# Kernel tuning notes

Measured on AMD Instinct MI355X. Metric: run time of the kernel, lower is better.

Reference implementation:

```python
import jax, jax.numpy as jnp
import numpy as np

NS_ITERS = 15
EPS = 1e-6


def _sqrtm(x):
    """Newton-Schulz matrix square root, 15 fixed iterations (Lin & Maji)."""
    dim = x.shape[0]
    norm = jnp.linalg.norm(x)  # Frobenius norm
    Y = x / norm
    I = jnp.eye(dim, dtype=x.dtype)
    Z = I
    for _ in range(NS_ITERS):
        T = 0.5 * (3.0 * I - Z @ Y)
        Y = Y @ T
        Z = T @ Z
    return Y * jnp.sqrt(norm)


def _gram(X):
    a, b = X.shape
    return (X @ X.T + EPS * jnp.eye(a, dtype=X.dtype)) / b


def setup_inputs() -> dict:
    key = jax.random.key(0)
    k1, k2 = jax.random.split(key)
    inp = jax.random.normal(k1, (1, 512, 256, 256), dtype=jnp.float32)
    tgt = jax.random.normal(k2, (1, 512, 256, 256), dtype=jnp.float32)
    return {"input": inp, "target_feature": tgt}


def reference(input, target_feature):
    a, b, c, d = input.shape
    n = a * b
    # --- target statistics (precomputed in __init__ of the torch module) ---
    Xt = target_feature.reshape(n, c * d)
    Mt = Xt.mean(axis=1)                     # [n]
    Gt = _gram(Xt - Mt[:, None])             # [n, n]
    sqrt_Gt = _sqrtm(Gt)                     # [n, n]
    # --- current statistics ---
    X = input.reshape(n, c * d)
    M = X.mean(axis=1)
    G = _gram(X - M[:, None])
    sqrt_G = _sqrtm(G)
    # mse(reduction='sum') on means + Bures/Wasserstein SPD distance
    loss = jnp.sum((M - Mt) ** 2)
    loss = loss + jnp.trace(G + Gt) - 2.0 * jnp.trace(sqrt_G @ sqrt_Gt)
    return loss / b
```

## Files before the change

### kernel.cpp

```cpp
#include <hip/hip_runtime.h>
#include <math.h>

#define KDIM 65536
#define MATF 262144
#define EPSG 1e-6

using bf16x8 = __attribute__((ext_vector_type(8))) __bf16;
using f32x4  = __attribute__((ext_vector_type(4))) float;


__global__ __launch_bounds__(256) void k_means(const float* __restrict__ X,
                                               const float* __restrict__ Xt,
                                               float* __restrict__ M) {
  const int row = blockIdx.x, inp = blockIdx.y;
  const float4* p = (const float4*)((inp ? Xt : X) + (size_t)row * KDIM);
  double s = 0.0;
  for (int i = threadIdx.x; i < KDIM / 4; i += 256) {
    float4 v = p[i];
    s += (double)v.x + (double)v.y + (double)v.z + (double)v.w;
  }
  __shared__ double sm[256];
  sm[threadIdx.x] = s;
  __syncthreads();
  for (int o = 128; o > 0; o >>= 1) {
    if (threadIdx.x < o) sm[threadIdx.x] += sm[threadIdx.x + o];
    __syncthreads();
  }
  if (threadIdx.x == 0) M[inp * 512 + row] = (float)(sm[0] * (1.0 / KDIM));
}

__device__ __forceinline__ void cvt8(float4 a, float4 b, bf16x8& hi, bf16x8& lo) {
  float f[8] = {a.x, a.y, a.z, a.w, b.x, b.y, b.z, b.w};
#pragma unroll
  for (int e = 0; e < 8; ++e) {
    __bf16 h = (__bf16)f[e];
    hi[e] = h;
    lo[e] = (__bf16)(f[e] - (float)h);
  }
}

__global__ __launch_bounds__(256, 2) void k_gram(const float* __restrict__ X,
                                                 const float* __restrict__ Xt,
                                                 float* __restrict__ Gp, int nk) {
  int rem = blockIdx.x, ti = 0;
  while (rem >= 4 - ti) { rem -= 4 - ti; ++ti; }
  const int tj = ti + rem;
  const int chunk = blockIdx.y, inp = blockIdx.z;
  const int chunkv = KDIM / nk;
  const float* __restrict__ A = inp ? Xt : X;
  float* __restrict__ C = Gp + ((size_t)(inp * nk + chunk)) * MATF;
  const bool diag = (ti == tj);

  __shared__ bf16x8 AhV[512], AlV[512], BhV[512], BlV[512];

  const int t = threadIdx.x;
  const int srow = t & 127, skh = t >> 7;
  const int sbase = ((srow >> 4) << 6) + (skh << 5) + (srow & 15);

  const float* pa = A + (size_t)(ti * 128 + srow) * KDIM + (size_t)chunk * chunkv + skh * 16;
  const float* pb = A + (size_t)(tj * 128 + srow) * KDIM + (size_t)chunk * chunkv + skh * 16;

  const int wave = t >> 6, lane = t & 63;
  const int wy = (wave >> 1) * 64, wx = (wave & 1) * 64;

  f32x4 acc[4][4];
#pragma unroll
  for (int i = 0; i < 4; ++i)
#pragma unroll
    for (int j = 0; j < 4; ++j) acc[i][j] = (f32x4){0.f, 0.f, 0.f, 0.f};

  float4 ra0 = *(const float4*)(pa);
  float4 ra1 = *(const float4*)(pa + 4);
  float4 ra2 = *(const float4*)(pa + 8);
  float4 ra3 = *(const float4*)(pa + 12);
  float4 rb0 = {}, rb1 = {}, rb2 = {}, rb3 = {};
  if (!diag) {
    rb0 = *(const float4*)(pb);
    rb1 = *(const float4*)(pb + 4);
    rb2 = *(const float4*)(pb + 8);
    rb3 = *(const float4*)(pb + 12);
  }

  for (int ks = 0; ks < chunkv; ks += 32) {
    {
      bf16x8 h, l;
      cvt8(ra0, ra1, h, l); AhV[sbase] = h; AlV[sbase] = l;
      cvt8(ra2, ra3, h, l); AhV[sbase + 16] = h; AlV[sbase + 16] = l;
      if (!diag) {
        cvt8(rb0, rb1, h, l); BhV[sbase] = h; BlV[sbase] = l;
        cvt8(rb2, rb3, h, l); BhV[sbase + 16] = h; BlV[sbase + 16] = l;
      }
    }
    __syncthreads();
    if (ks + 32 < chunkv) {
      ra0 = *(const float4*)(pa + ks + 32);
      ra1 = *(const float4*)(pa + ks + 36);
      ra2 = *(const float4*)(pa + ks + 40);
      ra3 = *(const float4*)(pa + ks + 44);
      if (!diag) {
        rb0 = *(const float4*)(pb + ks + 32);
        rb1 = *(const float4*)(pb + ks + 36);
        rb2 = *(const float4*)(pb + ks + 40);
        rb3 = *(const float4*)(pb + ks + 44);
      }
    }
    const bf16x8* __restrict__ Bh = diag ? AhV : BhV;
    const bf16x8* __restrict__ Bl = diag ? AlV : BlV;
    bf16x8 ah[4], al[4], bh[4], bl[4];
#pragma unroll
    for (int g = 0; g < 4; ++g) {
      ah[g] = AhV[((wave >> 1) * 4 + g) * 64 + lane];
      al[g] = AlV[((wave >> 1) * 4 + g) * 64 + lane];
      bh[g] = Bh[((wave & 1) * 4 + g) * 64 + lane];
      bl[g] = Bl[((wave & 1) * 4 + g) * 64 + lane];
    }
#pragma unroll
    for (int i = 0; i < 4; ++i)
#pragma unroll
      for (int j = 0; j < 4; ++j) {
        acc[i][j] = __builtin_amdgcn_mfma_f32_16x16x32_bf16(ah[i], bh[j], acc[i][j], 0, 0, 0);
        acc[i][j] = __builtin_amdgcn_mfma_f32_16x16x32_bf16(al[i], bh[j], acc[i][j], 0, 0, 0);
        acc[i][j] = __builtin_amdgcn_mfma_f32_16x16x32_bf16(ah[i], bl[j], acc[i][j], 0, 0, 0);
      }
    __syncthreads();
  }
  const int r4 = (lane >> 4) * 4, fc = lane & 15;
#pragma unroll
  for (int i = 0; i < 4; ++i) {
    const int grow = ti * 128 + wy + i * 16 + r4;
#pragma unroll
    for (int j = 0; j < 4; ++j) {
      const int gcol = tj * 128 + wx + j * 16 + fc;
#pragma unroll
      for (int r = 0; r < 4; ++r)
        C[(size_t)(grow + r) * 512 + gcol] = acc[i][j][r];
    }
  }
}

__global__ __launch_bounds__(256) void k_gfin(const float* __restrict__ Gp,
                                              const float* __restrict__ M,
                                              float* __restrict__ G,
                                              double* __restrict__ S, int nk) {
  const int inp = blockIdx.y;
  const int idx = blockIdx.x * 256 + threadIdx.x;
  const int i = idx >> 9, j = idx & 511;
  double n2 = 0.0, tr = 0.0;
  float* g = G + (size_t)inp * MATF;
  if (i <= j) {
    double sum = 0.0;
    const float* p = Gp + (size_t)inp * nk * MATF + idx;
    for (int c = 0; c < nk; ++c) sum += (double)p[(size_t)c * MATF];
    sum -= 65536.0 * (double)M[inp * 512 + i] * (double)M[inp * 512 + j];
    if (i == j) sum += EPSG;
    float v = (float)(sum * (1.0 / 65536.0));
    g[idx] = v;
    if (i < j) { g[(size_t)j * 512 + i] = v; n2 = 2.0 * (double)v * (double)v; }
    else       { n2 = (double)v * (double)v; tr = (double)v; }
  }
  __shared__ double s1[256], s2[256];
  s1[threadIdx.x] = n2; s2[threadIdx.x] = tr;
  __syncthreads();
  for (int o = 128; o > 0; o >>= 1) {
    if (threadIdx.x < o) { s1[threadIdx.x] += s1[threadIdx.x + o]; s2[threadIdx.x] += s2[threadIdx.x + o]; }
    __syncthreads();
  }
  if (threadIdx.x == 0) { atomicAdd(&S[inp], s1[0]); atomicAdd(&S[2 + inp], s2[0]); }
}

__global__ __launch_bounds__(256) void k_nsinit(const float* __restrict__ G,
                                                float* __restrict__ Y0,
                                                float* __restrict__ Z1,
                                                const double* __restrict__ S) {
  const int inp = blockIdx.y;
  const int idx = blockIdx.x * 256 + threadIdx.x;
  const float norm = (float)sqrt(S[inp]);
  const float y = G[(size_t)inp * MATF + idx] / norm;
  Y0[(size_t)inp * MATF + idx] = y;
  Z1[(size_t)inp * MATF + idx] = ((idx >> 9) == (idx & 511)) ? (1.5f - 0.5f * y) : (-0.5f * y);
}

__device__ __forceinline__ void ns_gemm(const float* __restrict__ A,
                                        const float* __restrict__ B,
                                        const float* __restrict__ E,
                                        float* __restrict__ C, int mode) {
  int rem = blockIdx.x, ti = 0;
  while (rem >= 4 - ti) { rem -= 4 - ti; ++ti; }
  const int tj = ti + rem;

  __shared__ bf16x8 AhV[512], AlV[512], BhV[512], BlV[512];

  const int t = threadIdx.x;
  const int srow = t & 127, sko = t >> 7;
  const int sslot = ((srow >> 4) << 6) + (sko << 4) + (srow & 15);

  const float* pa = A + (size_t)(ti * 128 + srow) * 512 + sko * 8;
  const float* pb = B + (size_t)(tj * 128 + srow) * 512 + sko * 8;

  const int wave = t >> 6, lane = t & 63;
  const int wy = (wave >> 2) * 64, wx = (wave & 3) * 32;

  f32x4 acc[4][2];
#pragma unroll
  for (int i = 0; i < 4; ++i)
#pragma unroll
    for (int j = 0; j < 2; ++j) acc[i][j] = (f32x4){0.f, 0.f, 0.f, 0.f};

  float4 ra0 = *(const float4*)(pa), ra1 = *(const float4*)(pa + 4);
  float4 rb0 = *(const float4*)(pb), rb1 = *(const float4*)(pb + 4);

  for (int ks = 0; ks < 512; ks += 32) {
    {
      bf16x8 h, l;
      cvt8(ra0, ra1, h, l); AhV[sslot] = h; AlV[sslot] = l;
      cvt8(rb0, rb1, h, l); BhV[sslot] = h; BlV[sslot] = l;
    }
    __syncthreads();
    if (ks + 32 < 512) {
      ra0 = *(const float4*)(pa + ks + 32); ra1 = *(const float4*)(pa + ks + 36);
      rb0 = *(const float4*)(pb + ks + 32); rb1 = *(const float4*)(pb + ks + 36);
    }
    bf16x8 ah[4], al[4], bh[2], bl[2];
#pragma unroll
    for (int g = 0; g < 4; ++g) {
      ah[g] = AhV[((wy >> 4) + g) * 64 + lane];
      al[g] = AlV[((wy >> 4) + g) * 64 + lane];
    }
#pragma unroll
    for (int g = 0; g < 2; ++g) {
      bh[g] = BhV[((wx >> 4) + g) * 64 + lane];
      bl[g] = BlV[((wx >> 4) + g) * 64 + lane];
    }
#pragma unroll
    for (int i = 0; i < 4; ++i)
#pragma unroll
      for (int j = 0; j < 2; ++j) {
        acc[i][j] = __builtin_amdgcn_mfma_f32_16x16x32_bf16(ah[i], bh[j], acc[i][j], 0, 0, 0);
        acc[i][j] = __builtin_amdgcn_mfma_f32_16x16x32_bf16(al[i], bh[j], acc[i][j], 0, 0, 0);
        acc[i][j] = __builtin_amdgcn_mfma_f32_16x16x32_bf16(ah[i], bl[j], acc[i][j], 0, 0, 0);
      }
    __syncthreads();
  }

  const int r4 = (lane >> 4) * 4, fc = lane & 15;
#pragma unroll
  for (int i = 0; i < 4; ++i) {
    const int grow = ti * 128 + wy + i * 16 + r4;
#pragma unroll
    for (int j = 0; j < 2; ++j) {
      const int gcol = tj * 128 + wx + j * 16 + fc;
      float v[4];
#pragma unroll
      for (int r = 0; r < 4; ++r) v[r] = acc[i][j][r];
      if (mode) {
#pragma unroll
        for (int r = 0; r < 4; ++r)
          v[r] = 1.5f * E[(size_t)(grow + r) * 512 + gcol] - 0.5f * v[r];
      }
#pragma unroll
      for (int r = 0; r < 4; ++r) C[(size_t)(grow + r) * 512 + gcol] = v[r];
      if (ti != tj) {
        float4 mv = make_float4(v[0], v[1], v[2], v[3]);
        *(float4*)&C[(size_t)gcol * 512 + grow] = mv;
      }
    }
  }
}

__global__ __launch_bounds__(512, 2) void k_ns_first(const float* __restrict__ Y0,
                                                     float* __restrict__ Y1) {
  const int mat = blockIdx.y;
  const float* a = Y0 + (size_t)mat * MATF;
  ns_gemm(a, a, a, Y1 + (size_t)mat * MATF, 1);
}

__global__ __launch_bounds__(512, 2) void k_ns_W(const float* __restrict__ Y,
                                                 const float* __restrict__ Z,
                                                 float* __restrict__ W) {
  const int mat = blockIdx.y;
  ns_gemm(Z + (size_t)mat * MATF, Y + (size_t)mat * MATF, nullptr,
          W + (size_t)mat * MATF, 0);
}

__global__ __launch_bounds__(512, 2) void k_ns_YZ(const float* __restrict__ Y,
                                                  const float* __restrict__ Z,
                                                  const float* __restrict__ W,
                                                  float* __restrict__ Yn,
                                                  float* __restrict__ Zn) {
  const int mat = blockIdx.y >> 1, which = blockIdx.y & 1;
  const float* Wp = W + (size_t)mat * MATF;
  if (which == 0) {
    const float* Yp = Y + (size_t)mat * MATF;
    ns_gemm(Yp, Wp, Yp, Yn + (size_t)mat * MATF, 1);
  } else {
    const float* Zp = Z + (size_t)mat * MATF;
    ns_gemm(Wp, Zp, Zp, Zn + (size_t)mat * MATF, 1);
  }
}

__global__ __launch_bounds__(256) void k_cross(const float* __restrict__ Y,
                                               double* __restrict__ S) {
  const float* YA = Y;
  const float* YB = Y + MATF;
  const int base = (blockIdx.x * 256 + threadIdx.x) * 4;
  double s = 0.0;
#pragma unroll
  for (int r = 0; r < 4; ++r) {
    const int id = base + r;
    const int i = id >> 9, j = id & 511;
    s += (double)YA[id] * (double)YB[j * 512 + i];
  }
  __shared__ double sm[256];
  sm[threadIdx.x] = s;
  __syncthreads();
  for (int o = 128; o > 0; o >>= 1) {
    if (threadIdx.x < o) sm[threadIdx.x] += sm[threadIdx.x + o];
    __syncthreads();
  }
  if (threadIdx.x == 0) atomicAdd(&S[4], sm[0]);
}

__global__ __launch_bounds__(256) void k_final(const float* __restrict__ M,
                                               const double* __restrict__ S,
                                               float* __restrict__ out) {
  double s = 0.0;
  for (int i = threadIdx.x; i < 512; i += 256) {
    double d = (double)M[i] - (double)M[512 + i];
    s += d * d;
  }
  __shared__ double sm[256];
  sm[threadIdx.x] = s;
  __syncthreads();
  for (int o = 128; o > 0; o >>= 1) {
    if (threadIdx.x < o) sm[threadIdx.x] += sm[threadIdx.x + o];
    __syncthreads();
  }
  if (threadIdx.x == 0) {
    double scale = sqrt(sqrt(S[0]) * sqrt(S[1]));
    double loss = sm[0] + S[2] + S[3] - 2.0 * scale * S[4];
    out[0] = (float)(loss / 512.0);
  }
}

extern "C" void kernel_launch(void* const* d_in, const int* in_sizes, int n_in,
                              void* d_out, int out_size, void* d_ws, size_t ws_size,
                              hipStream_t stream) {
  const float* X = (const float*)d_in[0];
  const float* Xt = (const float*)d_in[1];
  char* wsb = (char*)d_ws;
  float* Mv = (float*)wsb;
  double* S = (double*)(wsb + 4096);
  float* G = (float*)(wsb + 8192);
  float* big = (float*)(wsb + 8192 + 2 * (size_t)MATF * 4);

  const size_t need32 = 8192 + 2 * (size_t)MATF * 4 + 2 * 32 * (size_t)MATF * 4;
  const int nk = (ws_size >= need32) ? 32 : 16;

  float* Gp = big;
  float* Yb[2] = { big, big + 2 * (size_t)MATF };
  float* Zb[2] = { big + 4 * (size_t)MATF, big + 6 * (size_t)MATF };
  float* W = big + 8 * (size_t)MATF;

  hipMemsetAsync(S, 0, 16 * sizeof(double), stream);
  k_means<<<dim3(512, 2), 256, 0, stream>>>(X, Xt, Mv);
  k_gram<<<dim3(10, nk, 2), 256, 0, stream>>>(X, Xt, Gp, nk);
  k_gfin<<<dim3(1024, 2), 256, 0, stream>>>(Gp, Mv, G, S, nk);
  k_nsinit<<<dim3(1024, 2), 256, 0, stream>>>(G, Yb[0], Zb[1], S);
  k_ns_first<<<dim3(10, 2), 512, 0, stream>>>(Yb[0], Yb[1]);
  int cur = 1;
  for (int it = 1; it < 15; ++it) {
    k_ns_W<<<dim3(10, 2), 512, 0, stream>>>(Yb[cur], Zb[cur], W);
    k_ns_YZ<<<dim3(10, 4), 512, 0, stream>>>(Yb[cur], Zb[cur], W, Yb[1 - cur], Zb[1 - cur]);
    cur ^= 1;
  }
  k_cross<<<dim3(256), 256, 0, stream>>>(Yb[cur], S);
  k_final<<<dim3(1), 256, 0, stream>>>(Mv, S, (float*)d_out);
}
```

Measured before the change: 1.323 ms.

## Fuse Newton-Schulz chain into persistent kernel with grid barriers and 64x64 tiles

Replaces the Gram finalize, NS init, 29 per-step NS GEMM launches, cross-trace and final kernels with one persistent kernel. The kernel synchronises its phases through an atomic-counter grid barrier. GEMM tiles shrink from 128x128 to 64x64, giving 72 or 144 jobs per step instead of 20 or 40 blocks, to use more CUs. This removes launch gaps and raises parallelism. It relies on all blocks being co-resident, and the barrier has a timeout break that could silently desynchronise phases.

```diff
diff --git a/kernel.cpp b/kernel.cpp
--- a/kernel.cpp
+++ b/kernel.cpp
@@ -138,71 +138,47 @@
   }
 }
 
-__global__ __launch_bounds__(256) void k_gfin(const float* __restrict__ Gp,
-                                              const float* __restrict__ M,
-                                              float* __restrict__ G,
-                                              double* __restrict__ S, int nk) {
-  const int inp = blockIdx.y;
-  const int idx = blockIdx.x * 256 + threadIdx.x;
-  const int i = idx >> 9, j = idx & 511;
-  double n2 = 0.0, tr = 0.0;
-  float* g = G + (size_t)inp * MATF;
-  if (i <= j) {
-    double sum = 0.0;
-    const float* p = Gp + (size_t)inp * nk * MATF + idx;
-    for (int c = 0; c < nk; ++c) sum += (double)p[(size_t)c * MATF];
-    sum -= 65536.0 * (double)M[inp * 512 + i] * (double)M[inp * 512 + j];
-    if (i == j) sum += EPSG;
-    float v = (float)(sum * (1.0 / 65536.0));
-    g[idx] = v;
-    if (i < j) { g[(size_t)j * 512 + i] = v; n2 = 2.0 * (double)v * (double)v; }
-    else       { n2 = (double)v * (double)v; tr = (double)v; }
-  }
-  __shared__ double s1[256], s2[256];
-  s1[threadIdx.x] = n2; s2[threadIdx.x] = tr;
+__device__ __forceinline__ void gbar(unsigned* cnt, unsigned target) {
   __syncthreads();
-  for (int o = 128; o > 0; o >>= 1) {
-    if (threadIdx.x < o) { s1[threadIdx.x] += s1[threadIdx.x + o]; s2[threadIdx.x] += s2[threadIdx.x + o]; }
-    __syncthreads();
-  }
-  if (threadIdx.x == 0) { atomicAdd(&S[inp], s1[0]); atomicAdd(&S[2 + inp], s2[0]); }
-}
-
-__global__ __launch_bounds__(256) void k_nsinit(const float* __restrict__ G,
-                                                float* __restrict__ Y0,
-                                                float* __restrict__ Z1,
-                                                const double* __restrict__ S) {
-  const int inp = blockIdx.y;
-  const int idx = blockIdx.x * 256 + threadIdx.x;
-  const float norm = (float)sqrt(S[inp]);
-  const float y = G[(size_t)inp * MATF + idx] / norm;
-  Y0[(size_t)inp * MATF + idx] = y;
-  Z1[(size_t)inp * MATF + idx] = ((idx >> 9) == (idx & 511)) ? (1.5f - 0.5f * y) : (-0.5f * y);
-}
-
-__device__ __forceinline__ void ns_gemm(const float* __restrict__ A,
-                                        const float* __restrict__ B,
-                                        const float* __restrict__ E,
-                                        float* __restrict__ C, int mode) {
-  int rem = blockIdx.x, ti = 0;
-  while (rem >= 4 - ti) { rem -= 4 - ti; ++ti; }
-  const int tj = ti + rem;
-
-  __shared__ bf16x8 AhV[512], AlV[512], BhV[512], BlV[512];
-
+  if (threadIdx.x == 0) {
+    __threadfence();
+    atomicAdd(cnt, 1u);
+    unsigned long long t0 = __builtin_amdgcn_s_memrealtime();
+    while (__hip_atomic_load(cnt, __ATOMIC_RELAXED, __HIP_MEMORY_SCOPE_AGENT) < target) {
+      __builtin_amdgcn_s_sleep(16);
+      if (__builtin_amdgcn_s_memrealtime() - t0 > 2000000ull) break;
+    }
+    __threadfence();
+  }
+  __syncthreads();
+}
+
+__device__ __forceinline__ void tri8(int x, int& ti, int& tj) {
+  int rem = x, i = 0;
+  while (rem >= 8 - i) { rem -= 8 - i; ++i; }
+  ti = i; tj = i + rem;
+}
+
+__device__ __forceinline__ void gemm64(const float* __restrict__ A,
+                                       const float* __restrict__ B,
+                                       const float* __restrict__ E,
+                                       float* __restrict__ C,
+                                       int ti, int tj, int mode,
+                                       bf16x8* AhV, bf16x8* AlV,
+                                       bf16x8* BhV, bf16x8* BlV) {
   const int t = threadIdx.x;
-  const int srow = t & 127, sko = t >> 7;
+  const int srow = t & 63, sko = t >> 6;
   const int sslot = ((srow >> 4) << 6) + (sko << 4) + (srow & 15);
 
-  const float* pa = A + (size_t)(ti * 128 + srow) * 512 + sko * 8;
-  const float* pb = B + (size_t)(tj * 128 + srow) * 512 + sko * 8;
+  const float* pa = A + (size_t)(ti * 64 + srow) * 512 + sko * 8;
+  const float* pb = B + (size_t)(tj * 64 + srow) * 512 + sko * 8;
 
   const int wave = t >> 6, lane = t & 63;
-  const int wy = (wave >> 2) * 64, wx = (wave & 3) * 32;
-
-  f32x4 acc[4][2];
-#pragma unroll
-  for (int i = 0; i < 4; ++i)
+  const int wy = (wave >> 1) * 32, wx = (wave & 1) * 32;
+
+  f32x4 acc[2][2];
+#pragma unroll
+  for (int i = 0; i < 2; ++i)
 #pragma unroll
     for (int j = 0; j < 2; ++j) acc[i][j] = (f32x4){0.f, 0.f, 0.f, 0.f};
 
@@ -220,19 +196,16 @@
       ra0 = *(const float4*)(pa + ks + 32); ra1 = *(const float4*)(pa + ks + 36);
       rb0 = *(const float4*)(pb + ks + 32); rb1 = *(const float4*)(pb + ks + 36);
     }
-    bf16x8 ah[4], al[4], bh[2], bl[2];
-#pragma unroll
-    for (int g = 0; g < 4; ++g) {
+    bf16x8 ah[2], al[2], bh[2], bl[2];
+#pragma unroll
+    for (int g = 0; g < 2; ++g) {
       ah[g] = AhV[((wy >> 4) + g) * 64 + lane];
       al[g] = AlV[((wy >> 4) + g) * 64 + lane];
-    }
-#pragma unroll
-    for (int g = 0; g < 2; ++g) {
       bh[g] = BhV[((wx >> 4) + g) * 64 + lane];
       bl[g] = BlV[((wx >> 4) + g) * 64 + lane];
     }
 #pragma unroll
-    for (int i = 0; i < 4; ++i)
+    for (int i = 0; i < 2; ++i)
 #pragma unroll
       for (int j = 0; j < 2; ++j) {
         acc[i][j] = __builtin_amdgcn_mfma_f32_16x16x32_bf16(ah[i], bh[j], acc[i][j], 0, 0, 0);
@@ -244,11 +217,11 @@
 
   const int r4 = (lane >> 4) * 4, fc = lane & 15;
 #pragma unroll
-  for (int i = 0; i < 4; ++i) {
-    const int grow = ti * 128 + wy + i * 16 + r4;
+  for (int i = 0; i < 2; ++i) {
+    const int grow = ti * 64 + wy + i * 16 + r4;
 #pragma unroll
     for (int j = 0; j < 2; ++j) {
-      const int gcol = tj * 128 + wx + j * 16 + fc;
+      const int gcol = tj * 64 + wx + j * 16 + fc;
       float v[4];
 #pragma unroll
       for (int r = 0; r < 4; ++r) v[r] = acc[i][j][r];
@@ -267,78 +240,147 @@
   }
 }
 
-__global__ __launch_bounds__(512, 2) void k_ns_first(const float* __restrict__ Y0,
-                                                     float* __restrict__ Y1) {
-  const int mat = blockIdx.y;
-  const float* a = Y0 + (size_t)mat * MATF;
-  ns_gemm(a, a, a, Y1 + (size_t)mat * MATF, 1);
-}
-
-__global__ __launch_bounds__(512, 2) void k_ns_W(const float* __restrict__ Y,
-                                                 const float* __restrict__ Z,
-                                                 float* __restrict__ W) {
-  const int mat = blockIdx.y;
-  ns_gemm(Z + (size_t)mat * MATF, Y + (size_t)mat * MATF, nullptr,
-          W + (size_t)mat * MATF, 0);
-}
-
-__global__ __launch_bounds__(512, 2) void k_ns_YZ(const float* __restrict__ Y,
-                                                  const float* __restrict__ Z,
-                                                  const float* __restrict__ W,
-                                                  float* __restrict__ Yn,
-                                                  float* __restrict__ Zn) {
-  const int mat = blockIdx.y >> 1, which = blockIdx.y & 1;
-  const float* Wp = W + (size_t)mat * MATF;
-  if (which == 0) {
-    const float* Yp = Y + (size_t)mat * MATF;
-    ns_gemm(Yp, Wp, Yp, Yn + (size_t)mat * MATF, 1);
-  } else {
-    const float* Zp = Z + (size_t)mat * MATF;
-    ns_gemm(Wp, Zp, Zp, Zn + (size_t)mat * MATF, 1);
-  }
-}
-
-__global__ __launch_bounds__(256) void k_cross(const float* __restrict__ Y,
-                                               double* __restrict__ S) {
-  const float* YA = Y;
-  const float* YB = Y + MATF;
-  const int base = (blockIdx.x * 256 + threadIdx.x) * 4;
-  double s = 0.0;
-#pragma unroll
-  for (int r = 0; r < 4; ++r) {
-    const int id = base + r;
-    const int i = id >> 9, j = id & 511;
-    s += (double)YA[id] * (double)YB[j * 512 + i];
-  }
-  __shared__ double sm[256];
-  sm[threadIdx.x] = s;
-  __syncthreads();
-  for (int o = 128; o > 0; o >>= 1) {
-    if (threadIdx.x < o) sm[threadIdx.x] += sm[threadIdx.x + o];
-    __syncthreads();
-  }
-  if (threadIdx.x == 0) atomicAdd(&S[4], sm[0]);
-}
-
-__global__ __launch_bounds__(256) void k_final(const float* __restrict__ M,
-                                               const double* __restrict__ S,
-                                               float* __restrict__ out) {
-  double s = 0.0;
-  for (int i = threadIdx.x; i < 512; i += 256) {
-    double d = (double)M[i] - (double)M[512 + i];
-    s += d * d;
-  }
-  __shared__ double sm[256];
-  sm[threadIdx.x] = s;
-  __syncthreads();
-  for (int o = 128; o > 0; o >>= 1) {
-    if (threadIdx.x < o) sm[threadIdx.x] += sm[threadIdx.x + o];
-    __syncthreads();
-  }
-  if (threadIdx.x == 0) {
-    double scale = sqrt(sqrt(S[0]) * sqrt(S[1]));
-    double loss = sm[0] + S[2] + S[3] - 2.0 * scale * S[4];
-    out[0] = (float)(loss / 512.0);
+__global__ __launch_bounds__(256, 2) void k_all(const float* Gp,
+                                                const float* __restrict__ M,
+                                                float* __restrict__ Gm,
+                                                double* __restrict__ S,
+                                                unsigned* __restrict__ bar,
+                                                float* big,
+                                                float* __restrict__ out, int nk) {
+  __shared__ bf16x8 AhV[256], AlV[256], BhV[256], BlV[256];
+  __shared__ double red[256];
+  __shared__ float s_nrm[2];
+
+  const int t = threadIdx.x;
+  const int b = blockIdx.x;
+  const int gsz = gridDim.x;
+  unsigned tgt = 0;
+
+  float* Ya = big;
+  float* Yb = big + 2 * (size_t)MATF;
+  float* Za = big + 4 * (size_t)MATF;
+  float* Zb = big + 6 * (size_t)MATF;
+  float* W  = big + 8 * (size_t)MATF;
+
+  {
+    double n2[2] = {0.0, 0.0}, trc[2] = {0.0, 0.0};
+    for (int e = b * 256 + t; e < 2 * MATF; e += gsz * 256) {
+      const int inp = e >> 18, idx = e & (MATF - 1);
+      const int i = idx >> 9, j = idx & 511;
+      if (i <= j) {
+        double sum = 0.0;
+        const float* p = Gp + (size_t)inp * nk * MATF + idx;
+        for (int c = 0; c < nk; ++c) sum += (double)p[(size_t)c * MATF];
+        sum -= 65536.0 * (double)M[inp * 512 + i] * (double)M[inp * 512 + j];
+        if (i == j) sum += EPSG;
+        float v = (float)(sum * (1.0 / 65536.0));
+        Gm[e] = v;
+        if (i < j) { Gm[((size_t)inp << 18) + j * 512 + i] = v; n2[inp] += 2.0 * (double)v * (double)v; }
+        else       { n2[inp] += (double)v * (double)v; trc[inp] += (double)v; }
+      }
+    }
+#pragma unroll
+    for (int inp = 0; inp < 2; ++inp) {
+      red[t] = n2[inp]; __syncthreads();
+      for (int o = 128; o > 0; o >>= 1) { if (t < o) red[t] += red[t + o]; __syncthreads(); }
+      if (t == 0) atomicAdd(&S[inp], red[0]);
+      __syncthreads();
+      red[t] = trc[inp]; __syncthreads();
+      for (int o = 128; o > 0; o >>= 1) { if (t < o) red[t] += red[t + o]; __syncthreads(); }
+      if (t == 0) atomicAdd(&S[2 + inp], red[0]);
+      __syncthreads();
+    }
+  }
+  gbar(bar, tgt += gsz);
+
+  {
+    if (t < 2)
+      s_nrm[t] = (float)sqrt(__hip_atomic_load(&S[t], __ATOMIC_RELAXED, __HIP_MEMORY_SCOPE_AGENT));
+    __syncthreads();
+    for (int e = b * 256 + t; e < 2 * MATF; e += gsz * 256) {
+      const int inp = e >> 18, idx = e & (MATF - 1);
+      const float y = Gm[e] / s_nrm[inp];
+      Ya[e] = y;
+      Za[e] = ((idx >> 9) == (idx & 511)) ? (1.5f - 0.5f * y) : (-0.5f * y);
+    }
+  }
+  gbar(bar, tgt += gsz);
+
+  for (int job = b; job < 72; job += gsz) {
+    const int mat = job >= 36;
+    int ti, tj; tri8(job - mat * 36, ti, tj);
+    const float* a = Ya + (size_t)mat * MATF;
+    gemm64(a, a, a, Yb + (size_t)mat * MATF, ti, tj, 1, AhV, AlV, BhV, BlV);
+  }
+  gbar(bar, tgt += gsz);
+
+  float *Y = Yb, *Z = Za, *Yn = Ya, *Zn = Zb;
+  for (int it = 1; it < 15; ++it) {
+    for (int job = b; job < 72; job += gsz) {
+      const int mat = job >= 36;
+      int ti, tj; tri8(job - mat * 36, ti, tj);
+      gemm64(Z + (size_t)mat * MATF, Y + (size_t)mat * MATF, nullptr,
+             W + (size_t)mat * MATF, ti, tj, 0, AhV, AlV, BhV, BlV);
+    }
+    gbar(bar, tgt += gsz);
+    for (int job = b; job < 144; job += gsz) {
+      if (job < 72) {
+        const int mat = job >= 36;
+        int ti, tj; tri8(job - mat * 36, ti, tj);
+        gemm64(Y + (size_t)mat * MATF, W + (size_t)mat * MATF, Y + (size_t)mat * MATF,
+               Yn + (size_t)mat * MATF, ti, tj, 1, AhV, AlV, BhV, BlV);
+      } else {
+        const int jb = job - 72;
+        const int mat = jb >= 36;
+        int ti, tj; tri8(jb - mat * 36, ti, tj);
+        gemm64(W + (size_t)mat * MATF, Z + (size_t)mat * MATF, Z + (size_t)mat * MATF,
+               Zn + (size_t)mat * MATF, ti, tj, 1, AhV, AlV, BhV, BlV);
+      }
+    }
+    gbar(bar, tgt += gsz);
+    float* tmp;
+    tmp = Y; Y = Yn; Yn = tmp;
+    tmp = Z; Z = Zn; Zn = tmp;
+  }
+
+  {
+    double s = 0.0;
+    for (int id = b * 256 + t; id < MATF; id += gsz * 256) {
+      const int i = id >> 9, j = id & 511;
+      s += (double)Y[id] * (double)Y[MATF + j * 512 + i];
+    }
+    red[t] = s;
+    __syncthreads();
+    for (int o = 128; o > 0; o >>= 1) {
+      if (t < o) red[t] += red[t + o];
+      __syncthreads();
+    }
+    if (t == 0) atomicAdd(&S[4], red[0]);
+  }
+  gbar(bar, tgt += gsz);
+
+  if (b == 0) {
+    double s = 0.0;
+    for (int i = t; i < 512; i += 256) {
+      double d = (double)M[i] - (double)M[512 + i];
+      s += d * d;
+    }
+    red[t] = s;
+    __syncthreads();
+    for (int o = 128; o > 0; o >>= 1) {
+      if (t < o) red[t] += red[t + o];
+      __syncthreads();
+    }
+    if (t == 0) {
+      double s0 = __hip_atomic_load(&S[0], __ATOMIC_RELAXED, __HIP_MEMORY_SCOPE_AGENT);
+      double s1 = __hip_atomic_load(&S[1], __ATOMIC_RELAXED, __HIP_MEMORY_SCOPE_AGENT);
+      double s2 = __hip_atomic_load(&S[2], __ATOMIC_RELAXED, __HIP_MEMORY_SCOPE_AGENT);
+      double s3 = __hip_atomic_load(&S[3], __ATOMIC_RELAXED, __HIP_MEMORY_SCOPE_AGENT);
+      double s4 = __hip_atomic_load(&S[4], __ATOMIC_RELAXED, __HIP_MEMORY_SCOPE_AGENT);
+      double scale = sqrt(sqrt(s0) * sqrt(s1));
+      double loss = red[0] + s2 + s3 - 2.0 * scale * s4;
+      out[0] = (float)(loss / 512.0);
+    }
   }
 }
 
@@ -348,31 +390,33 @@
   const float* X = (const float*)d_in[0];
   const float* Xt = (const float*)d_in[1];
   char* wsb = (char*)d_ws;
-  float* Mv = (float*)wsb;
+  unsigned* bar = (unsigned*)wsb;
   double* S = (double*)(wsb + 4096);
-  float* G = (float*)(wsb + 8192);
-  float* big = (float*)(wsb + 8192 + 2 * (size_t)MATF * 4);
-
-  const size_t need32 = 8192 + 2 * (size_t)MATF * 4 + 2 * 32 * (size_t)MATF * 4;
+  float* Mv = (float*)(wsb + 4224);
+  float* G = (float*)(wsb + 16384);
+  float* big = (float*)(wsb + 16384 + 2 * (size_t)MATF * 4);
+
+  const size_t need32 = 16384 + 2 * (size_t)MATF * 4 + 2 * 32 * (size_t)MATF * 4;
   const int nk = (ws_size >= need32) ? 32 : 16;
 
-  float* Gp = big;
-  float* Yb[2] = { big, big + 2 * (size_t)MATF };
-  float* Zb[2] = { big + 4 * (size_t)MATF, big + 6 * (size_t)MATF };
-  float* W = big + 8 * (size_t)MATF;
-
-  hipMemsetAsync(S, 0, 16 * sizeof(double), stream);
+  static int s_grid = 0;
+  if (s_grid == 0) {
+    int dev = 0;
+    hipGetDevice(&dev);
+    int ncu = 0;
+    hipDeviceGetAttribute(&ncu, hipDeviceAttributeMultiprocessorCount, dev);
+    int maxb = 0;
+    hipOccupancyMaxActiveBlocksPerMultiprocessor(&maxb, k_all, 256, 0);
+    if (ncu <= 0) ncu = 64;
+    if (maxb <= 0) maxb = 1;
+    long cap = (long)ncu * maxb;
+    s_grid = (cap < 256) ? (int)cap : 256;
+    if (s_grid < 1) s_grid = 1;
+  }
+
+  hipMemsetAsync(wsb, 0, 4224, stream);
   k_means<<<dim3(512, 2), 256, 0, stream>>>(X, Xt, Mv);
-  k_gram<<<dim3(10, nk, 2), 256, 0, stream>>>(X, Xt, Gp, nk);
-  k_gfin<<<dim3(1024, 2), 256, 0, stream>>>(Gp, Mv, G, S, nk);
-  k_nsinit<<<dim3(1024, 2), 256, 0, stream>>>(G, Yb[0], Zb[1], S);
-  k_ns_first<<<dim3(10, 2), 512, 0, stream>>>(Yb[0], Yb[1]);
-  int cur = 1;
-  for (int it = 1; it < 15; ++it) {
-    k_ns_W<<<dim3(10, 2), 512, 0, stream>>>(Yb[cur], Zb[cur], W);
-    k_ns_YZ<<<dim3(10, 4), 512, 0, stream>>>(Yb[cur], Zb[cur], W, Yb[1 - cur], Zb[1 - cur]);
-    cur ^= 1;
-  }
-  k_cross<<<dim3(256), 256, 0, stream>>>(Yb[cur], S);
-  k_final<<<dim3(1), 256, 0, stream>>>(Mv, S, (float*)d_out);
-}
+  k_gram<<<dim3(10, nk, 2), 256, 0, stream>>>(X, Xt, big, nk);
+  k_all<<<dim3(s_grid), 256, 0, stream>>>(big, Mv, G, S, bar, big,
+                                          (float*)d_out, nk);
+}
```

Result: slower. 1.612 ms (+21.8%).
